# Kernel optimization log

Hardware: AMD Instinct MI355X
Metric: run time of the kernel (lower is better)

The kernel has to match this reference:

```python
import jax, jax.numpy as jnp
import numpy as np
from jax import lax

B, T, E, H, L, V = 32, 1024, 256, 512, 3, 10000
EPS = 1e-3  # Keras BatchNormalization default epsilon


def setup_inputs() -> dict:
    key = jax.random.key(0)
    ks = jax.random.split(key, 12)
    s = 0.05
    x = jax.random.randint(ks[0], (B, T), 0, V)
    emb = jax.random.normal(ks[1], (V, E), jnp.float32) * s
    k0 = jax.random.normal(ks[2], (E, 3 * H), jnp.float32) * s
    rk0 = jax.random.normal(ks[3], (H, 3 * H), jnp.float32) * s
    b0 = jax.random.normal(ks[4], (2, 3 * H), jnp.float32) * s
    krest = jax.random.normal(ks[5], (L - 1, H, 3 * H), jnp.float32) * s
    rkrest = jax.random.normal(ks[6], (L - 1, H, 3 * H), jnp.float32) * s
    brest = jax.random.normal(ks[7], (L - 1, 2, 3 * H), jnp.float32) * s
    gammas = jnp.ones((L, H), jnp.float32)
    betas = jnp.zeros((L, H), jnp.float32)
    return {"x": x, "emb": emb, "k0": k0, "rk0": rk0, "b0": b0,
            "krest": krest, "rkrest": rkrest, "brest": brest,
            "gammas": gammas, "betas": betas}


def _gru_layer(x_seq, h0, kernel, rkernel, bias):
    # Keras GRU, reset_after=True, activation=relu, recurrent_activation=sigmoid
    bi, br = bias[0], bias[1]
    xproj = jnp.einsum('bte,eh->bth', x_seq, kernel) + bi  # [B,T,3H]

    def step(h, xp):
        inner = h @ rkernel + br
        xz, xr, xh = jnp.split(xp, 3, axis=-1)
        hz, hr, hh = jnp.split(inner, 3, axis=-1)
        z = jax.nn.sigmoid(xz + hz)
        r = jax.nn.sigmoid(xr + hr)
        cand = jax.nn.relu(xh + r * hh)
        h_new = z * h + (1.0 - z) * cand
        return h_new, h_new

    hT, ys = lax.scan(step, h0, jnp.swapaxes(xproj, 0, 1))  # scan over T
    return jnp.swapaxes(ys, 0, 1), hT  # [B,T,H], [B,H]


def _batchnorm(y, gamma, beta):
    # training-mode BN over (batch, time), channel axis last
    mean = jnp.mean(y, axis=(0, 1))
    var = jnp.var(y, axis=(0, 1))
    return gamma * (y - mean) * lax.rsqrt(var + EPS) + beta


def reference(x, emb, k0, rk0, b0, krest, rkrest, brest, gammas, betas):
    h = jnp.zeros((B, H), jnp.float32)  # stateful GRU after reset_states()
    y = emb[x]  # [B,T,E] embedding lookup
    y, state = _gru_layer(y, h, k0, rk0, b0)
    y = _batchnorm(y, gammas[0], betas[0])
    for i in range(L - 1):  # subsequent layers get previous layer's state
        y, state = _gru_layer(y, state, krest[i], rkrest[i], brest[i])
        y = _batchnorm(y, gammas[i + 1], betas[i + 1])
    return y, state
```

## Files before the change

kernel.cpp:

```cpp
#include <hip/hip_runtime.h>
#include <hip/hip_bf16.h>

#define BB 32
#define TT 1024
#define EE 256
#define HH 512
#define H3 1536
#define MM (BB*TT)
#define NWG 16
#define EPS_BN 1e-3f

typedef __attribute__((ext_vector_type(8))) short bf16x8;
typedef __attribute__((ext_vector_type(4))) float f32x4;

__device__ __forceinline__ unsigned short f2bf(float f){
  unsigned u = __float_as_uint(f);
  u += 0x7fffu + ((u>>16)&1u);
  return (unsigned short)(u>>16);
}
__device__ __forceinline__ float bf2f(unsigned short u){
  return __uint_as_float(((unsigned)u)<<16);
}
__device__ __forceinline__ uint4 ld16_coh(const void* p){
  uint4 r;
  asm volatile("global_load_dwordx4 %0, %1, off sc0 sc1" : "=v"(r) : "v"(p) : "memory");
  return r;
}
__device__ __forceinline__ void st8_coh(void* p, uint2 v){
  asm volatile("global_store_dwordx2 %0, %1, off sc0 sc1" :: "v"(p), "v"(v) : "memory");
}

__global__ __launch_bounds__(256) void conv_transpose(
    const float* __restrict__ in, unsigned short* __restrict__ out, int K, int N){
  __shared__ float tile[32][33];
  int k0 = blockIdx.x*32, n0 = blockIdx.y*32;
  int tx = threadIdx.x & 31, ty = threadIdx.x >> 5;
  for(int i=ty;i<32;i+=8) tile[i][tx] = in[(size_t)(k0+i)*N + n0 + tx];
  __syncthreads();
  for(int i=ty;i<32;i+=8) out[(size_t)(n0+i)*K + k0 + tx] = f2bf(tile[tx][i]);
}

__global__ __launch_bounds__(256) void gather_emb(
    const int* __restrict__ x, const float* __restrict__ emb,
    unsigned short* __restrict__ y0){
  int i = blockIdx.x*256 + threadIdx.x;
  if(i >= MM*EE/4) return;
  int row = i >> 6;
  int c4 = (i & 63) << 2;
  int t = row >> 5, b = row & 31;
  float4 v = *(const float4*)&emb[(size_t)x[b*TT + t]*EE + c4];
  ushort4 o; o.x=f2bf(v.x); o.y=f2bf(v.y); o.z=f2bf(v.z); o.w=f2bf(v.w);
  *(ushort4*)&y0[(size_t)row*EE + c4] = o;
}

__global__ __launch_bounds__(256) void gemm_bias(
    const unsigned short* __restrict__ A,
    const unsigned short* __restrict__ BT,
    const float* __restrict__ bias,
    float* __restrict__ C, int Mdim, int Ndim, int Kdim){
  __shared__ __align__(16) unsigned short sA[64][72];
  __shared__ __align__(16) unsigned short sB[64][72];
  int m0 = blockIdx.x*64, n0 = blockIdx.y*64;
  int tid = threadIdx.x, ln = tid & 63, wv = tid >> 6;
  int wm = wv >> 1, wn = wv & 1;
  f32x4 acc[2][2] = {};
  for(int k0=0;k0<Kdim;k0+=64){
    __syncthreads();
    for(int p2=0;p2<2;p2++){
      int idx = (p2*256 + tid)*8;
      int r = idx >> 6, c = idx & 63;
      *(uint4*)&sA[r][c] = *(const uint4*)&A[(size_t)(m0+r)*Kdim + k0 + c];
      *(uint4*)&sB[r][c] = *(const uint4*)&BT[(size_t)(n0+r)*Kdim + k0 + c];
    }
    __syncthreads();
    for(int kk=0;kk<64;kk+=32){
      int kf = kk + ((ln>>4)<<3);
      bf16x8 af[2], bfr[2];
      for(int i=0;i<2;i++){
        af[i]  = *(const bf16x8*)&sA[wm*32 + i*16 + (ln&15)][kf];
        bfr[i] = *(const bf16x8*)&sB[wn*32 + i*16 + (ln&15)][kf];
      }
      for(int mi=0;mi<2;mi++)
        for(int ni=0;ni<2;ni++)
          acc[mi][ni] = __builtin_amdgcn_mfma_f32_16x16x32_bf16(af[mi], bfr[ni], acc[mi][ni], 0,0,0);
    }
  }
  for(int mi=0;mi<2;mi++)
    for(int ni=0;ni<2;ni++){
      int gn = n0 + wn*32 + ni*16 + (ln&15);
      float bs = bias ? bias[gn] : 0.f;
      int gm0 = m0 + wm*32 + mi*16 + ((ln>>4)<<2);
      for(int r2=0;r2<4;r2++)
        C[(size_t)(gm0+r2)*Ndim + gn] = acc[mi][ni][r2] + bs;
    }
}

__global__ __launch_bounds__(256,1) void gru_scan(
    const float* __restrict__ xproj,
    const unsigned short* __restrict__ rkT,
    const float* __restrict__ br,
    float* __restrict__ hstate,
    unsigned short* __restrict__ ybf,
    float* __restrict__ stats,
    unsigned short* Hbuf,
    int* flags, int C, int wbase){
  __shared__ __align__(16) unsigned short hlds[16][520];
  __shared__ float sredA[4][16];
  __shared__ float sredQ[4][16];
  const int wg = blockIdx.x;
  const int cg = wg >> 1, bg = wg & 1;
  const int chbase = cg*64;
  const int tid = threadIdx.x, ln = tid & 63, wv = tid >> 6;
  const int q = ln >> 4, frow = ln & 15;
  const int b = bg*16 + frow;
  const int chb = chbase + wv*16 + (q<<2);
  const int wrow = chbase + wv*16 + frow;
  const int kofs = q << 3;

  bf16x8 wf[3][16];
  #pragma unroll
  for(int g=0; g<3; g++){
    const unsigned short* wsrc = &rkT[(size_t)(g*HH + wrow)*HH];
    #pragma unroll
    for(int kk=0; kk<16; kk++)
      wf[g][kk] = *(const bf16x8*)&wsrc[kk*32 + kofs];
  }
  const f32x4 brz4 = *(const f32x4*)&br[0*HH + chb];
  const f32x4 brr4 = *(const f32x4*)&br[1*HH + chb];
  const f32x4 brh4 = *(const f32x4*)&br[2*HH + chb];

  f32x4 hv = *(const f32x4*)&hstate[b*HH + chb];
  {
    uint2 o;
    o.x = ((unsigned)f2bf(hv[1])<<16) | f2bf(hv[0]);
    o.y = ((unsigned)f2bf(hv[3])<<16) | f2bf(hv[2]);
    st8_coh(&Hbuf[(size_t)b*HH + chb], o);
  }
  asm volatile("s_waitcnt vmcnt(0)" ::: "memory");
  __syncthreads();
  if(tid==0) __hip_atomic_store(&flags[wg*16], wbase+1, __ATOMIC_RELAXED, __HIP_MEMORY_SCOPE_AGENT);
  f32x4 as = {0,0,0,0}, aq = {0,0,0,0};

  for(int s=0; s<C; s++){
    const int par = s & 1;
    const float* xp = &xproj[(size_t)s*BB*H3 + (size_t)b*H3];
    f32x4 xz4 = *(const f32x4*)&xp[chb];
    f32x4 xr4 = *(const f32x4*)&xp[HH + chb];
    f32x4 xh4 = *(const f32x4*)&xp[2*HH + chb];
    if(wv==0){
      const int need = wbase + s + 1;
      int guard = 0; bool done = false;
      while(!done && guard < 200000){
        int v = (ln < 8) ? __hip_atomic_load(&flags[(ln*2+bg)*16], __ATOMIC_RELAXED, __HIP_MEMORY_SCOPE_AGENT)
                         : 0x7fffffff;
        done = __all(v >= need) != 0;
        guard++;
      }
    }
    __syncthreads();
    {
      const unsigned short* src = &Hbuf[(size_t)par*BB*HH + (size_t)bg*16*HH];
      uint4 hb[4];
      #pragma unroll
      for(int j=0;j<4;j++) hb[j] = ld16_coh(&src[(j*256 + tid)*8]);
      asm volatile("s_waitcnt vmcnt(0)" ::: "memory");
      #pragma unroll
      for(int j=0;j<4;j++){
        int i = (j*256 + tid)*8;
        *(uint4*)&hlds[i>>9][i&511] = hb[j];
      }
    }
    __syncthreads();
    f32x4 acc[3] = {};
    #pragma unroll
    for(int kk=0; kk<16; kk++){
      bf16x8 hf = *(const bf16x8*)&hlds[frow][kk*32 + kofs];
      acc[0] = __builtin_amdgcn_mfma_f32_16x16x32_bf16(wf[0][kk], hf, acc[0], 0,0,0);
      acc[1] = __builtin_amdgcn_mfma_f32_16x16x32_bf16(wf[1][kk], hf, acc[1], 0,0,0);
      acc[2] = __builtin_amdgcn_mfma_f32_16x16x32_bf16(wf[2][kk], hf, acc[2], 0,0,0);
    }
    #pragma unroll
    for(int r2=0;r2<4;r2++){
      float z  = 1.f/(1.f + __expf(-(xz4[r2] + acc[0][r2] + brz4[r2])));
      float rr = 1.f/(1.f + __expf(-(xr4[r2] + acc[1][r2] + brr4[r2])));
      float cd = fmaxf(xh4[r2] + rr*(acc[2][r2] + brh4[r2]), 0.f);
      float hn = z*hv[r2] + (1.f - z)*cd;
      hv[r2] = hn;
      as[r2] += hn; aq[r2] += hn*hn;
    }
    uint2 o;
    o.x = ((unsigned)f2bf(hv[1])<<16) | f2bf(hv[0]);
    o.y = ((unsigned)f2bf(hv[3])<<16) | f2bf(hv[2]);
    st8_coh(&Hbuf[((size_t)(1-par)*BB + b)*HH + chb], o);
    asm volatile("s_waitcnt vmcnt(0)" ::: "memory");
    __syncthreads();
    if(tid==0) __hip_atomic_store(&flags[wg*16], wbase+s+2, __ATOMIC_RELAXED, __HIP_MEMORY_SCOPE_AGENT);
    *(uint2*)&ybf[((size_t)s*BB + b)*HH + chb] = o;
  }
  *(f32x4*)&hstate[b*HH + chb] = hv;
  #pragma unroll
  for(int d=1; d<16; d<<=1){
    #pragma unroll
    for(int r2=0;r2<4;r2++){
      as[r2] += __shfl_xor(as[r2], d);
      aq[r2] += __shfl_xor(aq[r2], d);
    }
  }
  if(frow==0){
    #pragma unroll
    for(int r2=0;r2<4;r2++){
      sredA[wv][(q<<2)+r2] = as[r2];
      sredQ[wv][(q<<2)+r2] = aq[r2];
    }
  }
  __syncthreads();
  if(tid < 64){
    float* st = stats + (size_t)bg*2*HH;
    st[chbase + tid]      += sredA[tid>>4][tid&15];
    st[HH + chbase + tid] += sredQ[tid>>4][tid&15];
  }
}

__global__ void bn_prep(const float* __restrict__ stats,
                        const float* __restrict__ gamma, const float* __restrict__ beta,
                        float* __restrict__ scsh){
  int c = blockIdx.x*256 + threadIdx.x;
  if(c >= HH) return;
  const float inv = 1.f/(float)MM;
  float s0 = stats[c] + stats[2*HH + c];
  float q0 = stats[HH + c] + stats[3*HH + c];
  float mean = s0*inv;
  float var  = q0*inv - mean*mean;
  float s = gamma[c]*rsqrtf(var + EPS_BN);
  scsh[c] = s; scsh[HH+c] = beta[c] - mean*s;
}

__global__ __launch_bounds__(256) void kscale(
    const unsigned short* __restrict__ kT, const float* __restrict__ scsh,
    const float* __restrict__ bias, unsigned short* __restrict__ kTs,
    float* __restrict__ badj){
  int n = blockIdx.x*4 + (threadIdx.x >> 6);
  int ln = threadIdx.x & 63;
  int k = ln*8;
  uint4 v = *(const uint4*)&kT[(size_t)n*HH + k];
  unsigned short* pv = (unsigned short*)&v;
  unsigned short ov[8];
  float acc = 0.f;
  for(int j=0;j<8;j++){
    float f = bf2f(pv[j]);
    acc += scsh[HH + k + j] * f;
    ov[j] = f2bf(f * scsh[k + j]);
  }
  *(uint4*)&kTs[(size_t)n*HH + k] = *(uint4*)ov;
  for(int d=1; d<64; d<<=1) acc += __shfl_xor(acc, d);
  if(ln==0) badj[n] = bias[n] + acc;
}

__global__ __launch_bounds__(256) void final_out(
    const unsigned short* __restrict__ ybf, const float* __restrict__ scsh,
    float* __restrict__ out){
  int row = blockIdx.x*4 + (threadIdx.x >> 6);
  int ln = threadIdx.x & 63;
  int t = row >> 5, b = row & 31;
  int k = ln*8;
  uint4 v = *(const uint4*)&ybf[(size_t)row*HH + k];
  unsigned short* pv = (unsigned short*)&v;
  float o[8];
  for(int j=0;j<8;j++) o[j] = bf2f(pv[j])*scsh[k+j] + scsh[HH+k+j];
  float4* dst = (float4*)&out[((size_t)b*TT + t)*HH + k];
  dst[0] = make_float4(o[0],o[1],o[2],o[3]);
  dst[1] = make_float4(o[4],o[5],o[6],o[7]);
}

__global__ void copy_f32(const float* __restrict__ in, float* __restrict__ out, int n){
  int i = blockIdx.x*blockDim.x + threadIdx.x;
  if(i<n) out[i] = in[i];
}

extern "C" void kernel_launch(void* const* d_in, const int* in_sizes, int n_in,
                              void* d_out, int out_size, void* d_ws, size_t ws_size,
                              hipStream_t stream){
  const int*   x      = (const int*)d_in[0];
  const float* emb    = (const float*)d_in[1];
  const float* k0     = (const float*)d_in[2];
  const float* rk0    = (const float*)d_in[3];
  const float* b0     = (const float*)d_in[4];
  const float* krest  = (const float*)d_in[5];
  const float* rkrest = (const float*)d_in[6];
  const float* brest  = (const float*)d_in[7];
  const float* gammas = (const float*)d_in[8];
  const float* betas  = (const float*)d_in[9];
  float* out_y = (float*)d_out;
  float* out_state = out_y + (size_t)MM*HH;

  char* p = (char*)d_ws;
  auto alloc = [&](size_t bytes)->void*{ void* r = p; p += (bytes + 255) & ~(size_t)255; return r; };
  unsigned short* ybf  = (unsigned short*)alloc((size_t)MM*HH*2);
  unsigned short* y0bf = (unsigned short*)alloc((size_t)MM*EE*2);
  unsigned short* kT0  = (unsigned short*)alloc((size_t)H3*EE*2);
  unsigned short* kT1  = (unsigned short*)alloc((size_t)H3*HH*2);
  unsigned short* kT2  = (unsigned short*)alloc((size_t)H3*HH*2);
  unsigned short* rkT0 = (unsigned short*)alloc((size_t)H3*HH*2);
  unsigned short* rkT1 = (unsigned short*)alloc((size_t)H3*HH*2);
  unsigned short* rkT2 = (unsigned short*)alloc((size_t)H3*HH*2);
  unsigned short* kTs  = (unsigned short*)alloc((size_t)H3*HH*2);
  float* badj   = (float*)alloc(H3*4);
  float* scsh   = (float*)alloc(2*HH*4);
  float* stats  = (float*)alloc(2*2*HH*4);
  float* hstate = (float*)alloc((size_t)BB*HH*4);
  unsigned short* Hbuf = (unsigned short*)alloc((size_t)2*BB*HH*2);
  int* flags = (int*)alloc(NWG*16*4);
  size_t fixed_bytes = (size_t)(p - (char*)d_ws);

  int C = 64;
  const int cands[4] = {1024, 512, 256, 128};
  for(int i=0;i<4;i++){
    if(fixed_bytes + (size_t)cands[i]*BB*H3*4 <= ws_size){ C = cands[i]; break; }
  }
  float* xproj = (float*)alloc((size_t)C*BB*H3*4);
  const int NC = TT / C;

  hipMemsetAsync(flags, 0, NWG*16*4, stream);
  hipMemsetAsync(hstate, 0, (size_t)BB*HH*4, stream);

  conv_transpose<<<dim3(EE/32, H3/32), 256, 0, stream>>>(k0, kT0, EE, H3);
  conv_transpose<<<dim3(HH/32, H3/32), 256, 0, stream>>>(krest, kT1, HH, H3);
  conv_transpose<<<dim3(HH/32, H3/32), 256, 0, stream>>>(krest + (size_t)HH*H3, kT2, HH, H3);
  conv_transpose<<<dim3(HH/32, H3/32), 256, 0, stream>>>(rk0, rkT0, HH, H3);
  conv_transpose<<<dim3(HH/32, H3/32), 256, 0, stream>>>(rkrest, rkT1, HH, H3);
  conv_transpose<<<dim3(HH/32, H3/32), 256, 0, stream>>>(rkrest + (size_t)HH*H3, rkT2, HH, H3);
  gather_emb<<<(MM*EE/4 + 255)/256, 256, 0, stream>>>(x, emb, y0bf);

  for(int L=0; L<3; L++){
    hipMemsetAsync(stats, 0, 2*2*HH*4, stream);
    const unsigned short* A; const unsigned short* BT; const float* bias;
    const unsigned short* rk; const float* rbias; int Kd;
    if(L == 0){
      A = y0bf; BT = kT0; bias = b0; rk = rkT0; rbias = b0 + H3; Kd = EE;
    } else {
      const unsigned short* kTn = (L==1) ? kT1 : kT2;
      const float* bn_bias = (L==1) ? brest : brest + 2*H3;
      kscale<<<H3/4, 256, 0, stream>>>(kTn, scsh, bn_bias, kTs, badj);
      A = ybf; BT = kTs; bias = badj; Kd = HH;
      rk = (L==1) ? rkT1 : rkT2;
      rbias = (L==1) ? brest + H3 : brest + 3*H3;
    }
    for(int c=0;c<NC;c++){
      int t0 = c*C;
      gemm_bias<<<dim3(C*BB/64, H3/64), 256, 0, stream>>>(
          A + (size_t)t0*BB*Kd, BT, bias, xproj, C*BB, H3, Kd);
      gru_scan<<<NWG, 256, 0, stream>>>(
          xproj, rk, rbias, hstate, ybf + (size_t)t0*BB*HH,
          stats, Hbuf, flags, C, L*(TT+1) + t0);
    }
    bn_prep<<<2, 256, 0, stream>>>(stats, gammas + L*HH, betas + L*HH, scsh);
  }
  final_out<<<MM/4, 256, 0, stream>>>(ybf, scsh, out_y);
  copy_f32<<<64, 256, 0, stream>>>(hstate, out_state, BB*HH);
}
```

Baseline: 9.126 ms.

## Replace per-step flag handshake with sequence-tagged hidden-state words in GRU scan

```diff
diff --git a/kernel.cpp b/kernel.cpp
--- a/kernel.cpp
+++ b/kernel.cpp
@@ -9,9 +9,11 @@
 #define MM (BB*TT)
 #define NWG 16
 #define EPS_BN 1e-3f
+#define GUARD_ROUNDS 3000
 
 typedef __attribute__((ext_vector_type(8))) short bf16x8;
 typedef __attribute__((ext_vector_type(4))) float f32x4;
+typedef __attribute__((ext_vector_type(4))) unsigned int u32x4;
 
 __device__ __forceinline__ unsigned short f2bf(float f){
   unsigned u = __float_as_uint(f);
@@ -26,8 +28,8 @@
   asm volatile("global_load_dwordx4 %0, %1, off sc0 sc1" : "=v"(r) : "v"(p) : "memory");
   return r;
 }
-__device__ __forceinline__ void st8_coh(void* p, uint2 v){
-  asm volatile("global_store_dwordx2 %0, %1, off sc0 sc1" :: "v"(p), "v"(v) : "memory");
+__device__ __forceinline__ void st16_coh(void* p, u32x4 v){
+  asm volatile("global_store_dwordx4 %0, %1, off sc0 sc1" :: "v"(p), "v"(v) : "memory");
 }
 
 __global__ __launch_bounds__(256) void conv_transpose(
@@ -102,9 +104,11 @@
     float* __restrict__ hstate,
     unsigned short* __restrict__ ybf,
     float* __restrict__ stats,
-    unsigned short* Hbuf,
-    int* flags, int C, int wbase){
-  __shared__ __align__(16) unsigned short hlds[16][520];
+    unsigned int* Hbuf,
+    int C, int wbase){
+  __shared__ __align__(16) unsigned short hlds[2][16][520];
+  __shared__ int sok[2][4];
+  __shared__ int sgive;
   __shared__ float sredA[4][16];
   __shared__ float sredQ[4][16];
   const int wg = blockIdx.x;
@@ -116,6 +120,7 @@
   const int chb = chbase + wv*16 + (q<<2);
   const int wrow = chbase + wv*16 + frow;
   const int kofs = q << 3;
+  if(tid==0) sgive = 0;
 
   bf16x8 wf[3][16];
   #pragma unroll
@@ -131,15 +136,14 @@
 
   f32x4 hv = *(const f32x4*)&hstate[b*HH + chb];
   {
-    uint2 o;
-    o.x = ((unsigned)f2bf(hv[1])<<16) | f2bf(hv[0]);
-    o.y = ((unsigned)f2bf(hv[3])<<16) | f2bf(hv[2]);
-    st8_coh(&Hbuf[(size_t)b*HH + chb], o);
-  }
-  asm volatile("s_waitcnt vmcnt(0)" ::: "memory");
-  __syncthreads();
-  if(tid==0) __hip_atomic_store(&flags[wg*16], wbase+1, __ATOMIC_RELAXED, __HIP_MEMORY_SCOPE_AGENT);
+    unsigned tg = ((unsigned)wbase & 0xffffu) << 16;
+    u32x4 o;
+    o.x = tg | f2bf(hv[0]); o.y = tg | f2bf(hv[1]);
+    o.z = tg | f2bf(hv[2]); o.w = tg | f2bf(hv[3]);
+    st16_coh(&Hbuf[(size_t)b*HH + chb], o);
+  }
   f32x4 as = {0,0,0,0}, aq = {0,0,0,0};
+  int gup = 0, rc = 0;
 
   for(int s=0; s<C; s++){
     const int par = s & 1;
@@ -147,38 +151,53 @@
     f32x4 xz4 = *(const f32x4*)&xp[chb];
     f32x4 xr4 = *(const f32x4*)&xp[HH + chb];
     f32x4 xh4 = *(const f32x4*)&xp[2*HH + chb];
-    if(wv==0){
-      const int need = wbase + s + 1;
-      int guard = 0; bool done = false;
-      while(!done && guard < 200000){
-        int v = (ln < 8) ? __hip_atomic_load(&flags[(ln*2+bg)*16], __ATOMIC_RELAXED, __HIP_MEMORY_SCOPE_AGENT)
-                         : 0x7fffffff;
-        done = __all(v >= need) != 0;
-        guard++;
+    const unsigned expt = (unsigned)(wbase + s) & 0xffffu;
+    const unsigned int* src = &Hbuf[((size_t)par*BB + bg*16)*HH];
+    int round = 0;
+    for(;;){
+      uint4 ta[4], tb[4];
+      #pragma unroll
+      for(int p2=0;p2<4;p2++){
+        int wi = (p2*256 + tid)*8;
+        ta[p2] = ld16_coh(&src[wi]);
+        tb[p2] = ld16_coh(&src[wi+4]);
       }
-    }
-    __syncthreads();
-    {
-      const unsigned short* src = &Hbuf[(size_t)par*BB*HH + (size_t)bg*16*HH];
-      uint4 hb[4];
+      asm volatile("s_waitcnt vmcnt(0)" ::: "memory");
+      unsigned bad = 0;
       #pragma unroll
-      for(int j=0;j<4;j++) hb[j] = ld16_coh(&src[(j*256 + tid)*8]);
-      asm volatile("s_waitcnt vmcnt(0)" ::: "memory");
-      #pragma unroll
-      for(int j=0;j<4;j++){
-        int i = (j*256 + tid)*8;
-        *(uint4*)&hlds[i>>9][i&511] = hb[j];
+      for(int p2=0;p2<4;p2++){
+        bad |= (ta[p2].x>>16)^expt; bad |= (ta[p2].y>>16)^expt;
+        bad |= (ta[p2].z>>16)^expt; bad |= (ta[p2].w>>16)^expt;
+        bad |= (tb[p2].x>>16)^expt; bad |= (tb[p2].y>>16)^expt;
+        bad |= (tb[p2].z>>16)^expt; bad |= (tb[p2].w>>16)^expt;
+        uint4 ov;
+        ov.x = (ta[p2].x & 0xffffu) | (ta[p2].y << 16);
+        ov.y = (ta[p2].z & 0xffffu) | (ta[p2].w << 16);
+        ov.z = (tb[p2].x & 0xffffu) | (tb[p2].y << 16);
+        ov.w = (tb[p2].z & 0xffffu) | (tb[p2].w << 16);
+        int i = (p2*256 + tid)*8;
+        *(uint4*)&hlds[par][i>>9][i&511] = ov;
       }
-    }
-    __syncthreads();
+      int myok = (__all(bad == 0) != 0) || (round >= GUARD_ROUNDS) || gup;
+      if(ln==0) sok[rc&1][wv] = myok;
+      if(tid==0 && round >= GUARD_ROUNDS) sgive = 1;
+      __syncthreads();
+      int allok = sok[rc&1][0] & sok[rc&1][1] & sok[rc&1][2] & sok[rc&1][3];
+      rc++;
+      if(allok) break;
+      round++;
+    }
+    gup |= sgive;
     f32x4 acc[3] = {};
     #pragma unroll
     for(int kk=0; kk<16; kk++){
-      bf16x8 hf = *(const bf16x8*)&hlds[frow][kk*32 + kofs];
+      bf16x8 hf = *(const bf16x8*)&hlds[par][frow][kk*32 + kofs];
       acc[0] = __builtin_amdgcn_mfma_f32_16x16x32_bf16(wf[0][kk], hf, acc[0], 0,0,0);
       acc[1] = __builtin_amdgcn_mfma_f32_16x16x32_bf16(wf[1][kk], hf, acc[1], 0,0,0);
       acc[2] = __builtin_amdgcn_mfma_f32_16x16x32_bf16(wf[2][kk], hf, acc[2], 0,0,0);
     }
+    unsigned tg = ((unsigned)(wbase + s + 1) & 0xffffu) << 16;
+    u32x4 o;
     #pragma unroll
     for(int r2=0;r2<4;r2++){
       float z  = 1.f/(1.f + __expf(-(xz4[r2] + acc[0][r2] + brz4[r2])));
@@ -186,16 +205,12 @@
       float cd = fmaxf(xh4[r2] + rr*(acc[2][r2] + brh4[r2]), 0.f);
       float hn = z*hv[r2] + (1.f - z)*cd;
       hv[r2] = hn;
+      ((unsigned*)&o)[r2] = tg | f2bf(hn);
       as[r2] += hn; aq[r2] += hn*hn;
     }
-    uint2 o;
-    o.x = ((unsigned)f2bf(hv[1])<<16) | f2bf(hv[0]);
-    o.y = ((unsigned)f2bf(hv[3])<<16) | f2bf(hv[2]);
-    st8_coh(&Hbuf[((size_t)(1-par)*BB + b)*HH + chb], o);
-    asm volatile("s_waitcnt vmcnt(0)" ::: "memory");
-    __syncthreads();
-    if(tid==0) __hip_atomic_store(&flags[wg*16], wbase+s+2, __ATOMIC_RELAXED, __HIP_MEMORY_SCOPE_AGENT);
-    *(uint2*)&ybf[((size_t)s*BB + b)*HH + chb] = o;
+    st16_coh(&Hbuf[((size_t)(1-par)*BB + b)*HH + chb], o);
+    uint2 yo; yo.x = (o.x&0xffffu)|(o.y<<16); yo.y = (o.z&0xffffu)|(o.w<<16);
+    *(uint2*)&ybf[((size_t)s*BB + b)*HH + chb] = yo;
   }
   *(f32x4*)&hstate[b*HH + chb] = hv;
   #pragma unroll
@@ -308,8 +323,7 @@
   float* scsh   = (float*)alloc(2*HH*4);
   float* stats  = (float*)alloc(2*2*HH*4);
   float* hstate = (float*)alloc((size_t)BB*HH*4);
-  unsigned short* Hbuf = (unsigned short*)alloc((size_t)2*BB*HH*2);
-  int* flags = (int*)alloc(NWG*16*4);
+  unsigned int* Hbuf = (unsigned int*)alloc((size_t)2*BB*HH*4);
   size_t fixed_bytes = (size_t)(p - (char*)d_ws);
 
   int C = 64;
@@ -320,8 +334,7 @@
   float* xproj = (float*)alloc((size_t)C*BB*H3*4);
   const int NC = TT / C;
 
-  hipMemsetAsync(flags, 0, NWG*16*4, stream);
-  hipMemsetAsync(hstate, 0, (size_t)BB*HH*4, stream);
+  (void)hipMemsetAsync(hstate, 0, (size_t)BB*HH*4, stream);
 
   conv_transpose<<<dim3(EE/32, H3/32), 256, 0, stream>>>(k0, kT0, EE, H3);
   conv_transpose<<<dim3(HH/32, H3/32), 256, 0, stream>>>(krest, kT1, HH, H3);
@@ -332,7 +345,7 @@
   gather_emb<<<(MM*EE/4 + 255)/256, 256, 0, stream>>>(x, emb, y0bf);
 
   for(int L=0; L<3; L++){
-    hipMemsetAsync(stats, 0, 2*2*HH*4, stream);
+    (void)hipMemsetAsync(stats, 0, 2*2*HH*4, stream);
     const unsigned short* A; const unsigned short* BT; const float* bias;
     const unsigned short* rk; const float* rbias; int Kd;
     if(L == 0){
@@ -351,7 +364,7 @@
           A + (size_t)t0*BB*Kd, BT, bias, xproj, C*BB, H3, Kd);
       gru_scan<<<NWG, 256, 0, stream>>>(
           xproj, rk, rbias, hstate, ybf + (size_t)t0*BB*HH,
-          stats, Hbuf, flags, C, L*(TT+1) + t0);
+          stats, Hbuf, C, L*(TT+1) + t0);
     }
     bn_prep<<<2, 256, 0, stream>>>(stats, gammas + L*HH, betas + L*HH, scsh);
   }
```

Result: slower. 10.81 ms (+18.5%).

## Replace block-wide barrier wait with per-wave flag polling on owned h slices

Applied to the files above, without the earlier changes.

```diff
diff --git a/kernel.cpp b/kernel.cpp
--- a/kernel.cpp
+++ b/kernel.cpp
@@ -141,34 +141,37 @@
   if(tid==0) __hip_atomic_store(&flags[wg*16], wbase+1, __ATOMIC_RELAXED, __HIP_MEMORY_SCOPE_AGENT);
   f32x4 as = {0,0,0,0}, aq = {0,0,0,0};
 
+  const int cgA = 2*wv, cgB = 2*wv + 1;
+  const int srow = ln >> 2, soct = ln & 3;
+
   for(int s=0; s<C; s++){
     const int par = s & 1;
     const float* xp = &xproj[(size_t)s*BB*H3 + (size_t)b*H3];
     f32x4 xz4 = *(const f32x4*)&xp[chb];
     f32x4 xr4 = *(const f32x4*)&xp[HH + chb];
     f32x4 xh4 = *(const f32x4*)&xp[2*HH + chb];
-    if(wv==0){
+    {
       const int need = wbase + s + 1;
       int guard = 0; bool done = false;
       while(!done && guard < 200000){
-        int v = (ln < 8) ? __hip_atomic_load(&flags[(ln*2+bg)*16], __ATOMIC_RELAXED, __HIP_MEMORY_SCOPE_AGENT)
-                         : 0x7fffffff;
+        int v = 0x7fffffff;
+        if(ln < 2){
+          v = __hip_atomic_load(&flags[((2*wv + ln)*2 + bg)*16],
+                                __ATOMIC_RELAXED, __HIP_MEMORY_SCOPE_AGENT);
+        }
         done = __all(v >= need) != 0;
         guard++;
       }
-    }
-    __syncthreads();
-    {
-      const unsigned short* src = &Hbuf[(size_t)par*BB*HH + (size_t)bg*16*HH];
-      uint4 hb[4];
-      #pragma unroll
-      for(int j=0;j<4;j++) hb[j] = ld16_coh(&src[(j*256 + tid)*8]);
+      const unsigned short* srcb = &Hbuf[((size_t)par*BB + bg*16 + srow)*HH];
+      uint4 hA0 = ld16_coh(&srcb[cgA*64 + soct*8]);
+      uint4 hA1 = ld16_coh(&srcb[cgA*64 + (soct+4)*8]);
+      uint4 hB0 = ld16_coh(&srcb[cgB*64 + soct*8]);
+      uint4 hB1 = ld16_coh(&srcb[cgB*64 + (soct+4)*8]);
       asm volatile("s_waitcnt vmcnt(0)" ::: "memory");
-      #pragma unroll
-      for(int j=0;j<4;j++){
-        int i = (j*256 + tid)*8;
-        *(uint4*)&hlds[i>>9][i&511] = hb[j];
-      }
+      *(uint4*)&hlds[srow][cgA*64 + soct*8]     = hA0;
+      *(uint4*)&hlds[srow][cgA*64 + (soct+4)*8] = hA1;
+      *(uint4*)&hlds[srow][cgB*64 + soct*8]     = hB0;
+      *(uint4*)&hlds[srow][cgB*64 + (soct+4)*8] = hB1;
     }
     __syncthreads();
     f32x4 acc[3] = {};
@@ -320,8 +323,8 @@
   float* xproj = (float*)alloc((size_t)C*BB*H3*4);
   const int NC = TT / C;
 
-  hipMemsetAsync(flags, 0, NWG*16*4, stream);
-  hipMemsetAsync(hstate, 0, (size_t)BB*HH*4, stream);
+  (void)hipMemsetAsync(flags, 0, NWG*16*4, stream);
+  (void)hipMemsetAsync(hstate, 0, (size_t)BB*HH*4, stream);
 
   conv_transpose<<<dim3(EE/32, H3/32), 256, 0, stream>>>(k0, kT0, EE, H3);
   conv_transpose<<<dim3(HH/32, H3/32), 256, 0, stream>>>(krest, kT1, HH, H3);
@@ -332,7 +335,7 @@
   gather_emb<<<(MM*EE/4 + 255)/256, 256, 0, stream>>>(x, emb, y0bf);
 
   for(int L=0; L<3; L++){
-    hipMemsetAsync(stats, 0, 2*2*HH*4, stream);
+    (void)hipMemsetAsync(stats, 0, 2*2*HH*4, stream);
     const unsigned short* A; const unsigned short* BT; const float* bias;
     const unsigned short* rk; const float* rbias; int Kd;
     if(L == 0){
```

After: 9.165 ms (median of 2 runs). No clear change (+0.4%).

## Use per-wavefront flags and direct global h loads in GRU scan

Applied to the files above, without the earlier changes.

```diff
diff --git a/kernel.cpp b/kernel.cpp
--- a/kernel.cpp
+++ b/kernel.cpp
@@ -104,7 +104,6 @@
     float* __restrict__ stats,
     unsigned short* Hbuf,
     int* flags, int C, int wbase){
-  __shared__ __align__(16) unsigned short hlds[16][520];
   __shared__ float sredA[4][16];
   __shared__ float sredQ[4][16];
   const int wg = blockIdx.x;
@@ -116,6 +115,8 @@
   const int chb = chbase + wv*16 + (q<<2);
   const int wrow = chbase + wv*16 + frow;
   const int kofs = q << 3;
+  const int pollIdx = ((((ln>>2)*2 + bg)*4) + (ln&3))*16;
+  const int myFlag  = (wg*4 + wv)*16;
 
   bf16x8 wf[3][16];
   #pragma unroll
@@ -137,8 +138,7 @@
     st8_coh(&Hbuf[(size_t)b*HH + chb], o);
   }
   asm volatile("s_waitcnt vmcnt(0)" ::: "memory");
-  __syncthreads();
-  if(tid==0) __hip_atomic_store(&flags[wg*16], wbase+1, __ATOMIC_RELAXED, __HIP_MEMORY_SCOPE_AGENT);
+  if(ln==0) __hip_atomic_store(&flags[myFlag], wbase+1, __ATOMIC_RELAXED, __HIP_MEMORY_SCOPE_AGENT);
   f32x4 as = {0,0,0,0}, aq = {0,0,0,0};
 
   for(int s=0; s<C; s++){
@@ -147,54 +147,52 @@
     f32x4 xz4 = *(const f32x4*)&xp[chb];
     f32x4 xr4 = *(const f32x4*)&xp[HH + chb];
     f32x4 xh4 = *(const f32x4*)&xp[2*HH + chb];
-    if(wv==0){
+    {
       const int need = wbase + s + 1;
       int guard = 0; bool done = false;
-      while(!done && guard < 200000){
-        int v = (ln < 8) ? __hip_atomic_load(&flags[(ln*2+bg)*16], __ATOMIC_RELAXED, __HIP_MEMORY_SCOPE_AGENT)
+      while(!done && guard < 6000){
+        int v0 = (ln<32) ? __hip_atomic_load(&flags[pollIdx], __ATOMIC_RELAXED, __HIP_MEMORY_SCOPE_AGENT)
                          : 0x7fffffff;
-        done = __all(v >= need) != 0;
+        int v1 = (ln<32) ? __hip_atomic_load(&flags[pollIdx], __ATOMIC_RELAXED, __HIP_MEMORY_SCOPE_AGENT)
+                         : 0x7fffffff;
+        done = __all(v0 >= need) != 0;
+        if(!done) done = __all(v1 >= need) != 0;
         guard++;
       }
     }
-    __syncthreads();
-    {
-      const unsigned short* src = &Hbuf[(size_t)par*BB*HH + (size_t)bg*16*HH];
-      uint4 hb[4];
-      #pragma unroll
-      for(int j=0;j<4;j++) hb[j] = ld16_coh(&src[(j*256 + tid)*8]);
-      asm volatile("s_waitcnt vmcnt(0)" ::: "memory");
-      #pragma unroll
-      for(int j=0;j<4;j++){
-        int i = (j*256 + tid)*8;
-        *(uint4*)&hlds[i>>9][i&511] = hb[j];
-      }
-    }
-    __syncthreads();
-    f32x4 acc[3] = {};
+    const unsigned short* hsrc = &Hbuf[((size_t)par*BB + bg*16 + frow)*HH];
+    uint4 hb[16];
+    #pragma unroll
+    for(int kk=0; kk<16; kk++)
+      hb[kk] = ld16_coh(&hsrc[kk*32 + kofs]);
+    asm volatile("s_waitcnt vmcnt(0)" ::: "memory");
+    __builtin_amdgcn_sched_barrier(0);
+    f32x4 acc[3][2] = {};
     #pragma unroll
     for(int kk=0; kk<16; kk++){
-      bf16x8 hf = *(const bf16x8*)&hlds[frow][kk*32 + kofs];
-      acc[0] = __builtin_amdgcn_mfma_f32_16x16x32_bf16(wf[0][kk], hf, acc[0], 0,0,0);
-      acc[1] = __builtin_amdgcn_mfma_f32_16x16x32_bf16(wf[1][kk], hf, acc[1], 0,0,0);
-      acc[2] = __builtin_amdgcn_mfma_f32_16x16x32_bf16(wf[2][kk], hf, acc[2], 0,0,0);
-    }
+      union { uint4 u; bf16x8 v; } hf; hf.u = hb[kk];
+      acc[0][kk&1] = __builtin_amdgcn_mfma_f32_16x16x32_bf16(wf[0][kk], hf.v, acc[0][kk&1], 0,0,0);
+      acc[1][kk&1] = __builtin_amdgcn_mfma_f32_16x16x32_bf16(wf[1][kk], hf.v, acc[1][kk&1], 0,0,0);
+      acc[2][kk&1] = __builtin_amdgcn_mfma_f32_16x16x32_bf16(wf[2][kk], hf.v, acc[2][kk&1], 0,0,0);
+    }
+    uint2 o;
     #pragma unroll
     for(int r2=0;r2<4;r2++){
-      float z  = 1.f/(1.f + __expf(-(xz4[r2] + acc[0][r2] + brz4[r2])));
-      float rr = 1.f/(1.f + __expf(-(xr4[r2] + acc[1][r2] + brr4[r2])));
-      float cd = fmaxf(xh4[r2] + rr*(acc[2][r2] + brh4[r2]), 0.f);
+      float az = acc[0][0][r2] + acc[0][1][r2];
+      float ar = acc[1][0][r2] + acc[1][1][r2];
+      float ah = acc[2][0][r2] + acc[2][1][r2];
+      float z  = 1.f/(1.f + __expf(-(xz4[r2] + az + brz4[r2])));
+      float rr = 1.f/(1.f + __expf(-(xr4[r2] + ar + brr4[r2])));
+      float cd = fmaxf(xh4[r2] + rr*(ah + brh4[r2]), 0.f);
       float hn = z*hv[r2] + (1.f - z)*cd;
       hv[r2] = hn;
       as[r2] += hn; aq[r2] += hn*hn;
     }
-    uint2 o;
     o.x = ((unsigned)f2bf(hv[1])<<16) | f2bf(hv[0]);
     o.y = ((unsigned)f2bf(hv[3])<<16) | f2bf(hv[2]);
     st8_coh(&Hbuf[((size_t)(1-par)*BB + b)*HH + chb], o);
     asm volatile("s_waitcnt vmcnt(0)" ::: "memory");
-    __syncthreads();
-    if(tid==0) __hip_atomic_store(&flags[wg*16], wbase+s+2, __ATOMIC_RELAXED, __HIP_MEMORY_SCOPE_AGENT);
+    if(ln==0) __hip_atomic_store(&flags[myFlag], wbase+s+2, __ATOMIC_RELAXED, __HIP_MEMORY_SCOPE_AGENT);
     *(uint2*)&ybf[((size_t)s*BB + b)*HH + chb] = o;
   }
   *(f32x4*)&hstate[b*HH + chb] = hv;
@@ -309,7 +307,7 @@
   float* stats  = (float*)alloc(2*2*HH*4);
   float* hstate = (float*)alloc((size_t)BB*HH*4);
   unsigned short* Hbuf = (unsigned short*)alloc((size_t)2*BB*HH*2);
-  int* flags = (int*)alloc(NWG*16*4);
+  int* flags = (int*)alloc(NWG*4*16*4);
   size_t fixed_bytes = (size_t)(p - (char*)d_ws);
 
   int C = 64;
@@ -320,8 +318,8 @@
   float* xproj = (float*)alloc((size_t)C*BB*H3*4);
   const int NC = TT / C;
 
-  hipMemsetAsync(flags, 0, NWG*16*4, stream);
-  hipMemsetAsync(hstate, 0, (size_t)BB*HH*4, stream);
+  (void)hipMemsetAsync(flags, 0, NWG*4*16*4, stream);
+  (void)hipMemsetAsync(hstate, 0, (size_t)BB*HH*4, stream);
 
   conv_transpose<<<dim3(EE/32, H3/32), 256, 0, stream>>>(k0, kT0, EE, H3);
   conv_transpose<<<dim3(HH/32, H3/32), 256, 0, stream>>>(krest, kT1, HH, H3);
@@ -332,7 +330,7 @@
   gather_emb<<<(MM*EE/4 + 255)/256, 256, 0, stream>>>(x, emb, y0bf);
 
   for(int L=0; L<3; L++){
-    hipMemsetAsync(stats, 0, 2*2*HH*4, stream);
+    (void)hipMemsetAsync(stats, 0, 2*2*HH*4, stream);
     const unsigned short* A; const unsigned short* BT; const float* bias;
     const unsigned short* rk; const float* rbias; int Kd;
     if(L == 0){
```

After: 14.89 ms. 63.2% more time.
